# Optimization experiments

Measured on AMD Instinct MI355X. Metric: run time of the kernel, lower is better.

## Reference

```python
import jax, jax.numpy as jnp
import numpy as np

# model dims (see init_kwargs)
HID = 2048
H = 16
Q_LORA = 768
KV_LORA = 512
QK_NOPE = 128
QK_ROPE = 64
QK_HEAD = QK_NOPE + QK_ROPE  # 192
V_DIM = 128
HI = 8        # indexer heads
DI = 128      # indexer head dim
TOPK = 512    # index_topk
EPS = 1e-5
B, S = 1, 2048


def rms_norm(x, w):
    return x * jax.lax.rsqrt(jnp.mean(x * x, -1, keepdims=True) + EPS) * w


def layer_norm(x, w, b):
    m = jnp.mean(x, -1, keepdims=True)
    v = jnp.mean((x - m) ** 2, -1, keepdims=True)
    return (x - m) * jax.lax.rsqrt(v + EPS) * w + b


def rotate_half(x):
    x1, x2 = jnp.split(x, 2, axis=-1)
    return jnp.concatenate([-x2, x1], axis=-1)


def rope_bshd(x, cos, sin):
    # x: [B,S,H,D], cos/sin: [B,S,D] -> broadcast over heads (unsqueeze_dim=2)
    return x * cos[:, :, None, :] + rotate_half(x) * sin[:, :, None, :]


def setup_inputs() -> dict:
    key = jax.random.key(0)
    ks = jax.random.split(key, 16)
    std = 0.02
    hidden_states = jax.random.normal(ks[0], (B, S, HID), jnp.float32)
    # real RoPE tables, theta=10000, head_dim=QK_ROPE
    inv_freq = 1.0 / (10000.0 ** (np.arange(0, QK_ROPE, 2, dtype=np.float32) / QK_ROPE))
    freqs = np.arange(S, dtype=np.float32)[:, None] * inv_freq[None, :]  # [S, ROPE/2]
    emb = np.concatenate([freqs, freqs], axis=-1)
    cos = jnp.asarray(np.cos(emb))[None]  # [1,S,ROPE]
    sin = jnp.asarray(np.sin(emb))[None]
    w = lambda k, shp: jax.random.normal(k, shp, jnp.float32) * std
    return {
        'hidden_states': hidden_states, 'cos': cos, 'sin': sin,
        'wq_a': w(ks[1], (Q_LORA, HID)),
        'q_a_norm_w': jnp.ones((Q_LORA,), jnp.float32),
        'wq_b': w(ks[2], (H * QK_HEAD, Q_LORA)),
        'wkv_a': w(ks[3], (KV_LORA + QK_ROPE, HID)),
        'kv_a_norm_w': jnp.ones((KV_LORA,), jnp.float32),
        'wkv_b': w(ks[4], (H * (QK_NOPE + V_DIM), KV_LORA)),
        'wo': w(ks[5], (HID, H * V_DIM)),
        'idx_wq_b': w(ks[6], (HI * DI, Q_LORA)),
        'idx_wk': w(ks[7], (DI, HID)),
        'idx_k_norm_w': jnp.ones((DI,), jnp.float32),
        'idx_k_norm_b': jnp.zeros((DI,), jnp.float32),
        'idx_weights_w': w(ks[8], (HI, HID)),
    }


def reference(hidden_states, cos, sin, wq_a, q_a_norm_w, wq_b, wkv_a, kv_a_norm_w,
              wkv_b, wo, idx_wq_b, idx_wk, idx_k_norm_w, idx_k_norm_b, idx_weights_w):
    b, s, _ = hidden_states.shape
    # ---- MLA projections ----
    q_lora = rms_norm(hidden_states @ wq_a.T, q_a_norm_w)              # [B,S,Q_LORA]
    q = (q_lora @ wq_b.T).reshape(b, s, H, QK_HEAD)
    q_nope, q_rope = jnp.split(q, [QK_NOPE], axis=-1)
    q_rope = rope_bshd(q_rope, cos, sin)

    kv = hidden_states @ wkv_a.T                                        # [B,S,KV_LORA+ROPE]
    kv_lat, k_rope = jnp.split(kv, [KV_LORA], axis=-1)
    k_rope = k_rope * cos + rotate_half(k_rope) * sin                   # shared MQA rope key [B,S,ROPE]
    kv_lat = rms_norm(kv_lat, kv_a_norm_w)
    kvb = (kv_lat @ wkv_b.T).reshape(b, s, H, QK_NOPE + V_DIM)
    k_nope, value = jnp.split(kvb, [QK_NOPE], axis=-1)

    queries = jnp.concatenate([q_nope, q_rope], axis=-1)                # [B,S,H,QK_HEAD]
    keys = jnp.concatenate(
        [k_nope, jnp.broadcast_to(k_rope[:, :, None, :], (b, s, H, QK_ROPE))], axis=-1)

    # ---- lightning indexer (DSA): per-query top-k KV selection ----
    iq = (q_lora @ idx_wq_b.T).reshape(b, s, HI, DI)
    iq_rot, iq_pass = jnp.split(iq, [QK_ROPE], axis=-1)
    iq = jnp.concatenate([rope_bshd(iq_rot, cos, sin), iq_pass], axis=-1)
    ik = layer_norm(hidden_states @ idx_wk.T, idx_k_norm_w, idx_k_norm_b)  # [B,S,DI]
    ik_rot, ik_pass = jnp.split(ik, [QK_ROPE], axis=-1)
    ik = jnp.concatenate([ik_rot * cos + rotate_half(ik_rot) * sin, ik_pass], axis=-1)

    iscores = jnp.einsum('bqhd,bkd->bqhk', iq, ik) * (DI ** -0.5)       # [B,S,HI,S]
    iw = (hidden_states @ idx_weights_w.T) * (HI ** -0.5)               # [B,S,HI]
    iscore = jnp.einsum('bqh,bqhk->bqk', iw, iscores)                   # [B,S,S]

    causal = jnp.tril(jnp.ones((s, s), bool))
    iscore = jnp.where(causal[None], iscore, -1e9)
    _, topk_idx = jax.lax.top_k(iscore, TOPK)                           # [B,S,TOPK]
    allow = jnp.zeros((b, s, s), bool).at[
        jnp.arange(b)[:, None, None], jnp.arange(s)[None, :, None], topk_idx].set(True)
    allow = allow & causal[None]                                        # topk AND causal

    # ---- masked attention ----
    scale = QK_HEAD ** -0.5
    scores = jnp.einsum('bqhd,bkhd->bhqk', queries, keys) * scale       # [B,H,S,S]
    scores = jnp.where(allow[:, None], scores, -jnp.inf)
    probs = jax.nn.softmax(scores, axis=-1)
    out = jnp.einsum('bhqk,bkhd->bqhd', probs, value).reshape(b, s, H * V_DIM)
    return out @ wo.T
```

## Files before the change

kernel.cpp:

```cpp
#include <hip/hip_runtime.h>
#include <hip/hip_bf16.h>
#include <stdint.h>
#include <math.h>

#define S_LEN 2048
#define HIDDEN 2048
#define NHEAD 16
#define QLORA 768
#define KVLORA 512
#define QKNOPE 128
#define QKROPE 64
#define QKHEAD 192
#define VDIM 128
#define HIN 8
#define DIN 128
#define TOPKN 512
#define EPSF 1e-5f
#define DLAT 576
#define SCALE_ATT 0.07216878364870322f

typedef __bf16 bf16x8 __attribute__((ext_vector_type(8)));
typedef float  f32x4  __attribute__((ext_vector_type(4)));

static __device__ __forceinline__ float wave_reduce_sum(float v) {
    #pragma unroll
    for (int off = 32; off > 0; off >>= 1) v += __shfl_down(v, off);
    return v;
}

static __device__ __forceinline__ void splitw(__bf16* __restrict__ H,
                                              __bf16* __restrict__ L,
                                              size_t idx, float v) {
    __bf16 h = (__bf16)v;
    H[idx] = h;
    L[idx] = (__bf16)(v - (float)h);
}

static __device__ __forceinline__ void gll16(const __bf16* g, __bf16* lds_base) {
    __builtin_amdgcn_global_load_lds(
        (const __attribute__((address_space(1))) uint32_t*)g,
        (__attribute__((address_space(3))) uint32_t*)lds_base, 16, 0, 0);
}

#define PREP_BLOCKS 17280
__global__ __launch_bounds__(256) void prep_all(
        const float* __restrict__ hid,     __bf16* hidH,  __bf16* hidL,
        const float* __restrict__ wq_a,    __bf16* wqaH,  __bf16* wqaL,
        const float* __restrict__ idx_wq_b,__bf16* iwqH,  __bf16* iwqL,
        const float* __restrict__ idx_wk,  __bf16* iwkH,  __bf16* iwkL,
        const float* __restrict__ wq_b,    __bf16* wq_b_bf,
        const float* __restrict__ wkv_a,   __bf16* wkv_a_bf,
        const float* __restrict__ wkv_b,   __bf16* wkv_b_bf,
        const float* __restrict__ wo,      __bf16* wo_bf,
        __bf16* wknt) {
    int b = blockIdx.x, tid = threadIdx.x;
    const float* src; __bf16 *dH = nullptr, *dL = nullptr, *dC = nullptr;
    int base;
    if (b < 4096)        { src = hid;      dH = hidH; dL = hidL; base = b; }
    else if (b < 5632)   { src = wq_a;     dH = wqaH; dL = wqaL; base = b - 4096; }
    else if (b < 6400)   { src = idx_wq_b; dH = iwqH; dL = iwqL; base = b - 5632; }
    else if (b < 6656)   { src = idx_wk;   dH = iwkH; dL = iwkL; base = b - 6400; }
    else if (b < 8960)   { src = wq_b;     dC = wq_b_bf;  base = b - 6656; }
    else if (b < 10112)  { src = wkv_a;    dC = wkv_a_bf; base = b - 8960; }
    else if (b < 12160)  { src = wkv_b;    dC = wkv_b_bf; base = b - 10112; }
    else if (b < 16256)  { src = wo;       dC = wo_bf;    base = b - 12160; }
    else {
        int e = ((b - 16256) * 256 + tid) * 4;
        int c = e & 511, d = (e >> 9) & 127, h = e >> 16;
        f32x4 v = *(const f32x4*)(wkv_b + ((size_t)(h * 256 + d)) * 512 + c);
        #pragma unroll
        for (int j = 0; j < 4; ++j)
            wknt[(size_t)h * 65536 + (c + j) * 128 + d] = (__bf16)v[j];
        return;
    }
    int i = (base * 256 + tid) * 4;
    f32x4 v = *(const f32x4*)(src + i);
    if (dC) {
        #pragma unroll
        for (int j = 0; j < 4; ++j) dC[i + j] = (__bf16)v[j];
    } else {
        #pragma unroll
        for (int j = 0; j < 4; ++j) splitw(dH, dL, i + j, v[j]);
    }
}

#define GBM 128
#define GBN 64
#define GBK 32
template <typename OutT>
static __device__ __forceinline__ void gemm_s_core(
        const __bf16* __restrict__ A, const __bf16* __restrict__ B,
        OutT* __restrict__ C, int K, int lda, int ldb, int ldc,
        int bx, int by) {
    __shared__ __bf16 sAs[GBM * GBK];
    __shared__ __bf16 sBs[GBN * GBK];
    int tid = threadIdx.x;
    int lane = tid & 63, wid = tid >> 6;
    int quad = lane >> 4, l16 = lane & 15;
    int wm = wid >> 1, wn = wid & 1;
    int row0 = by * GBM, col0 = bx * GBN;
    int lr = lane >> 2, lk = (lane & 3) * 8;

    f32x4 acc[4][2] = {};

    for (int k0 = 0; k0 < K; k0 += GBK) {
        #pragma unroll
        for (int c = 0; c < 2; ++c) {
            int rb = (wid * 2 + c) * 16;
            gll16(A + (size_t)(row0 + rb + lr) * lda + k0 + lk, sAs + rb * GBK);
        }
        gll16(B + (size_t)(col0 + wid * 16 + lr) * ldb + k0 + lk, sBs + wid * 16 * GBK);
        __syncthreads();
        bf16x8 af[4], bfr[2];
        #pragma unroll
        for (int mi = 0; mi < 4; ++mi)
            af[mi] = *(const bf16x8*)&sAs[(wm * 64 + mi * 16 + l16) * GBK + quad * 8];
        #pragma unroll
        for (int ni = 0; ni < 2; ++ni)
            bfr[ni] = *(const bf16x8*)&sBs[(wn * 32 + ni * 16 + l16) * GBK + quad * 8];
        #pragma unroll
        for (int mi = 0; mi < 4; ++mi)
            #pragma unroll
            for (int ni = 0; ni < 2; ++ni)
                acc[mi][ni] = __builtin_amdgcn_mfma_f32_16x16x32_bf16(
                    af[mi], bfr[ni], acc[mi][ni], 0, 0, 0);
        __syncthreads();
    }
    #pragma unroll
    for (int mi = 0; mi < 4; ++mi)
        #pragma unroll
        for (int ni = 0; ni < 2; ++ni)
            #pragma unroll
            for (int r = 0; r < 4; ++r) {
                int row = row0 + wm * 64 + mi * 16 + quad * 4 + r;
                int col = col0 + wn * 32 + ni * 16 + l16;
                C[(size_t)row * ldc + col] = (OutT)acc[mi][ni][r];
            }
}

template <typename OutT>
__global__ __launch_bounds__(256) void gemm_s(const __bf16* __restrict__ A,
                                              const __bf16* __restrict__ B,
                                              OutT* __restrict__ C,
                                              int K, int lda, int ldb, int ldc,
                                              long sA, long sB, long sC) {
    gemm_s_core<OutT>(A + (size_t)blockIdx.z * sA, B + (size_t)blockIdx.z * sB,
                      C + (size_t)blockIdx.z * sC, K, lda, ldb, ldc,
                      blockIdx.x, blockIdx.y);
}

template <bool CAUSAL>
static __device__ __forceinline__ void gemm3_core(
        const __bf16* __restrict__ Ah, const __bf16* __restrict__ Al,
        const __bf16* __restrict__ Bh, const __bf16* __restrict__ Bl,
        float* __restrict__ C, int K, int lda, int ldb, int ldc,
        int row_base, int bx, int by) {
    int row0 = by * GBM + row_base, col0 = bx * GBN;
    if (CAUSAL && col0 > row0 + GBM - 1) return;
    __shared__ __bf16 sAh[GBM * GBK], sAl[GBM * GBK];
    __shared__ __bf16 sBh[GBN * GBK], sBl[GBN * GBK];
    int tid = threadIdx.x;
    int lane = tid & 63, wid = tid >> 6;
    int quad = lane >> 4, l16 = lane & 15;
    int wm = wid >> 1, wn = wid & 1;
    int lr = lane >> 2, lk = (lane & 3) * 8;

    f32x4 acc[4][2] = {};

    for (int k0 = 0; k0 < K; k0 += GBK) {
        #pragma unroll
        for (int c = 0; c < 2; ++c) {
            int rb = (wid * 2 + c) * 16;
            size_t go = (size_t)(row0 + rb + lr) * lda + k0 + lk;
            gll16(Ah + go, sAh + rb * GBK);
            gll16(Al + go, sAl + rb * GBK);
        }
        {
            size_t go = (size_t)(col0 + wid * 16 + lr) * ldb + k0 + lk;
            gll16(Bh + go, sBh + wid * 16 * GBK);
            gll16(Bl + go, sBl + wid * 16 * GBK);
        }
        __syncthreads();
        bf16x8 afh[4], afl[4], bfh[2], bfl[2];
        #pragma unroll
        for (int mi = 0; mi < 4; ++mi) {
            int o = (wm * 64 + mi * 16 + l16) * GBK + quad * 8;
            afh[mi] = *(const bf16x8*)&sAh[o];
            afl[mi] = *(const bf16x8*)&sAl[o];
        }
        #pragma unroll
        for (int ni = 0; ni < 2; ++ni) {
            int o = (wn * 32 + ni * 16 + l16) * GBK + quad * 8;
            bfh[ni] = *(const bf16x8*)&sBh[o];
            bfl[ni] = *(const bf16x8*)&sBl[o];
        }
        #pragma unroll
        for (int mi = 0; mi < 4; ++mi)
            #pragma unroll
            for (int ni = 0; ni < 2; ++ni) {
                acc[mi][ni] = __builtin_amdgcn_mfma_f32_16x16x32_bf16(
                    afl[mi], bfh[ni], acc[mi][ni], 0, 0, 0);
                acc[mi][ni] = __builtin_amdgcn_mfma_f32_16x16x32_bf16(
                    afh[mi], bfl[ni], acc[mi][ni], 0, 0, 0);
                acc[mi][ni] = __builtin_amdgcn_mfma_f32_16x16x32_bf16(
                    afh[mi], bfh[ni], acc[mi][ni], 0, 0, 0);
            }
        __syncthreads();
    }
    #pragma unroll
    for (int mi = 0; mi < 4; ++mi)
        #pragma unroll
        for (int ni = 0; ni < 2; ++ni)
            #pragma unroll
            for (int r = 0; r < 4; ++r) {
                int row = row0 + wm * 64 + mi * 16 + quad * 4 + r;
                int col = col0 + wn * 32 + ni * 16 + l16;
                C[(size_t)row * ldc + col] = acc[mi][ni][r];
            }
}

__global__ __launch_bounds__(256) void gemm3_ks(const __bf16* __restrict__ Ah,
                                                const __bf16* __restrict__ Al,
                                                const __bf16* __restrict__ Bh,
                                                const __bf16* __restrict__ Bl,
                                                float* __restrict__ Cpart,
                                                int Ksub, int lda, int ldb, int ldc,
                                                long sC) {
    int bz = blockIdx.z, koff = bz * Ksub;
    gemm3_core<false>(Ah + koff, Al + koff, Bh + koff, Bl + koff,
                      Cpart + (size_t)bz * sC, Ksub, lda, ldb, ldc, 0,
                      blockIdx.x, blockIdx.y);
}

__global__ __launch_bounds__(256) void fused_mid(
        const __bf16* __restrict__ qlH, const __bf16* __restrict__ qlL,
        const __bf16* __restrict__ wq_b_bf, __bf16* __restrict__ qbuf_bf,
        const __bf16* __restrict__ hidH, const __bf16* __restrict__ hidL,
        const __bf16* __restrict__ wkv_a_bf, float* __restrict__ kv,
        const __bf16* __restrict__ iwqH, const __bf16* __restrict__ iwqL,
        float* __restrict__ iqraw,
        const __bf16* __restrict__ iwkH, const __bf16* __restrict__ iwkL,
        float* __restrict__ ikraw) {
    int b = blockIdx.x;
    if (b < 768) {
        gemm_s_core<__bf16>(qlH, wq_b_bf, qbuf_bf, QLORA, QLORA, QLORA,
                            NHEAD * QKHEAD, b % 48, b / 48);
    } else if (b < 912) {
        int r = b - 768;
        gemm_s_core<float>(hidH, wkv_a_bf, kv, HIDDEN, HIDDEN, HIDDEN, DLAT,
                           r % 9, r / 9);
    } else if (b < 1168) {
        int r = b - 912;
        gemm3_core<false>(qlH, qlL, iwqH, iwqL, iqraw, QLORA, QLORA, QLORA,
                          HIN * DIN, 0, r & 15, r >> 4);
    } else {
        int r = b - 1168;
        gemm3_core<false>(hidH, hidL, iwkH, iwkL, ikraw, HIDDEN, HIDDEN, HIDDEN,
                          DIN, 0, r & 1, r >> 1);
    }
}

__global__ __launch_bounds__(256) void fused2(
        const __bf16* __restrict__ qbuf_bf, const __bf16* __restrict__ wknt,
        __bf16* __restrict__ qeff,
        const __bf16* __restrict__ cqH, const __bf16* __restrict__ cqL,
        const __bf16* __restrict__ ikH, const __bf16* __restrict__ ikL,
        float* __restrict__ iscore) {
    int b = blockIdx.x;
    if (b < 2048) {
        int bx = b & 7, by = (b >> 3) & 15, bz = b >> 7;
        gemm_s_core<__bf16>(qbuf_bf + bz * QKHEAD, wknt + (size_t)bz * 512 * 128,
                            qeff + bz * DLAT, 128, NHEAD * QKHEAD, 128,
                            NHEAD * DLAT, bx, by);
    } else {
        int r = b - 2048;
        gemm3_core<true>(cqH, cqL, ikH, ikL, iscore, DIN, DIN, DIN, S_LEN,
                         TOPKN, r & 31, r >> 5);
    }
}

__global__ __launch_bounds__(256) void rmsnorm_split4(const float* __restrict__ p,
                                                      long ps,
                                                      const float* __restrict__ w,
                                                      __bf16* __restrict__ yH,
                                                      __bf16* __restrict__ yL, int ncols) {
    int row = blockIdx.x, tid = threadIdx.x;
    const float* p0 = p + (size_t)row * ncols;
    float ss = 0.f;
    for (int c = tid; c < ncols; c += 256) {
        float v = p0[c] + p0[ps + c] + p0[2 * ps + c] + p0[3 * ps + c];
        ss += v * v;
    }
    __shared__ float red[4];
    ss = wave_reduce_sum(ss);
    if ((tid & 63) == 0) red[tid >> 6] = ss;
    __syncthreads();
    float tot = red[0] + red[1] + red[2] + red[3];
    float inv = rsqrtf(tot / (float)ncols + EPSF);
    for (int c = tid; c < ncols; c += 256) {
        float v = p0[c] + p0[ps + c] + p0[2 * ps + c] + p0[3 * ps + c];
        splitw(yH, yL, (size_t)row * ncols + c, v * inv * w[c]);
    }
}

__global__ __launch_bounds__(256) void fused_post(
        const __bf16* __restrict__ qbuf, __bf16* __restrict__ qeff,
        const float* __restrict__ kv, const float* __restrict__ kvw,
        __bf16* __restrict__ klat,
        const float* __restrict__ ikraw, const float* __restrict__ lnw,
        const float* __restrict__ lnb, __bf16* __restrict__ ikH, __bf16* __restrict__ ikL,
        const float* __restrict__ iqraw, const float* __restrict__ hid,
        const float* __restrict__ iww, __bf16* __restrict__ cqH, __bf16* __restrict__ cqL,
        const float* __restrict__ cosT, const float* __restrict__ sinT) {
    int s = blockIdx.x, tid = threadIdx.x;
    int lane = tid & 63, wid = tid >> 6;

    for (int i = tid; i < NHEAD * 32; i += 256) {
        int h = i >> 5, d = i & 31;
        const __bf16* base = qbuf + (size_t)s * (NHEAD * QKHEAD) + h * QKHEAD + QKNOPE;
        float x1 = (float)base[d], x2 = (float)base[d + 32];
        float c1 = cosT[s * 64 + d],      s1 = sinT[s * 64 + d];
        float c2 = cosT[s * 64 + d + 32], s2 = sinT[s * 64 + d + 32];
        __bf16* o = qeff + (size_t)s * (NHEAD * DLAT) + h * DLAT + 512;
        o[d]      = (__bf16)(x1 * c1 - x2 * s1);
        o[d + 32] = (__bf16)(x2 * c2 + x1 * s2);
    }

    {
        const float* row = kv + (size_t)s * DLAT;
        float ss = 0.f;
        for (int c = tid; c < KVLORA; c += 256) { float v = row[c]; ss += v * v; }
        __shared__ float redB[4];
        ss = wave_reduce_sum(ss);
        if (lane == 0) redB[wid] = ss;
        __syncthreads();
        float tot = redB[0] + redB[1] + redB[2] + redB[3];
        float inv = rsqrtf(tot / (float)KVLORA + EPSF);
        __bf16* orow = klat + (size_t)s * DLAT;
        for (int c = tid; c < KVLORA; c += 256)
            orow[c] = (__bf16)(row[c] * inv * kvw[c]);
        if (tid < 32) {
            int d = tid;
            float x1 = row[KVLORA + d], x2 = row[KVLORA + d + 32];
            float c1 = cosT[s * 64 + d],      s1 = sinT[s * 64 + d];
            float c2 = cosT[s * 64 + d + 32], s2 = sinT[s * 64 + d + 32];
            orow[512 + d]      = (__bf16)(x1 * c1 - x2 * s1);
            orow[512 + d + 32] = (__bf16)(x2 * c2 + x1 * s2);
        }
    }

    {
        float x = (tid < DIN) ? ikraw[(size_t)s * DIN + tid] : 0.f;
        __shared__ float redC1[4], redC2[4], sy[DIN];
        float sm = wave_reduce_sum(x);
        if (lane == 0) redC1[wid] = sm;
        __syncthreads();
        float mean = (redC1[0] + redC1[1] + redC1[2] + redC1[3]) / (float)DIN;
        float dx = (tid < DIN) ? (x - mean) : 0.f;
        float vs = wave_reduce_sum(dx * dx);
        if (lane == 0) redC2[wid] = vs;
        __syncthreads();
        float var = (redC2[0] + redC2[1] + redC2[2] + redC2[3]) / (float)DIN;
        if (tid < DIN) sy[tid] = dx * rsqrtf(var + EPSF) * lnw[tid] + lnb[tid];
        __syncthreads();
        size_t ro = (size_t)s * DIN;
        if (tid < 32) {
            int d = tid;
            float c1 = cosT[s * 64 + d],      s1 = sinT[s * 64 + d];
            float c2 = cosT[s * 64 + d + 32], s2 = sinT[s * 64 + d + 32];
            splitw(ikH, ikL, ro + d,      sy[d] * c1 - sy[d + 32] * s1);
            splitw(ikH, ikL, ro + d + 32, sy[d + 32] * c2 + sy[d] * s2);
        } else if (tid >= 64 && tid < DIN) {
            splitw(ikH, ikL, ro + tid, sy[tid]);
        }
        __syncthreads();
    }

    {
        __shared__ float redD[4][HIN], siw[HIN];
        float a8[HIN] = {};
        const float* xr = hid + (size_t)s * HIDDEN;
        for (int c = tid; c < HIDDEN; c += 256) {
            float x = xr[c];
            #pragma unroll
            for (int h = 0; h < HIN; ++h) a8[h] += x * iww[h * HIDDEN + c];
        }
        #pragma unroll
        for (int h = 0; h < HIN; ++h) a8[h] = wave_reduce_sum(a8[h]);
        if (lane == 0)
            #pragma unroll
            for (int h = 0; h < HIN; ++h) redD[wid][h] = a8[h];
        __syncthreads();
        if (tid < HIN)
            siw[tid] = redD[0][tid] + redD[1][tid] + redD[2][tid] + redD[3][tid];
        __syncthreads();
        if (tid < DIN) {
            int d = tid;
            float acc = 0.f;
            float c1 = 0.f, s1 = 0.f;
            if (d < 64) { c1 = cosT[s * 64 + d]; s1 = sinT[s * 64 + d]; }
            #pragma unroll
            for (int h = 0; h < HIN; ++h) {
                const float* base = iqraw + ((size_t)s * HIN + h) * DIN;
                float v;
                if (d < 32)       v = base[d] * c1 - base[d + 32] * s1;
                else if (d < 64)  v = base[d] * c1 + base[d - 32] * s1;
                else              v = base[d];
                acc += siw[h] * v;
            }
            splitw(cqH, cqL, (size_t)s * DIN + d, acc * 0.03125f);
        }
    }
}

__global__ __launch_bounds__(256) void topk_rows(const float* __restrict__ iscore,
                                                 int* __restrict__ topk) {
    int q = TOPKN + blockIdx.x;
    int n = q + 1;
    __shared__ uint32_t skey[S_LEN];
    __shared__ int hist[256];
    __shared__ int scan[256];
    __shared__ uint32_t sp;
    __shared__ int sr, pos;
    int tid = threadIdx.x;
    const float* row = iscore + (size_t)q * S_LEN;
    for (int i = tid; i < n; i += 256) {
        uint32_t u = __float_as_uint(row[i]);
        skey[i] = (u & 0x80000000u) ? ~u : (u | 0x80000000u);
    }
    __syncthreads();
    uint32_t prefix = 0;
    int remk = TOPKN;
    for (int pass = 0; pass < 4; ++pass) {
        int shift = 24 - 8 * pass;
        uint32_t pmask = pass ? (0xFFFFFFFFu << (shift + 8)) : 0u;
        hist[tid] = 0;
        __syncthreads();
        for (int i = tid; i < n; i += 256) {
            uint32_t u = skey[i];
            if ((u & pmask) == prefix) atomicAdd(&hist[(u >> shift) & 255], 1);
        }
        __syncthreads();
        scan[tid] = hist[tid];
        __syncthreads();
        for (int step = 1; step < 256; step <<= 1) {
            int v = (tid + step < 256) ? scan[tid + step] : 0;
            __syncthreads();
            scan[tid] += v;
            __syncthreads();
        }
        int Sb = scan[tid];
        int Snext = (tid < 255) ? scan[tid + 1] : 0;
        if (Sb >= remk && Snext < remk) {
            sp = prefix | ((uint32_t)tid << shift);
            sr = remk - Snext;
        }
        __syncthreads();
        prefix = sp; remk = sr;
        __syncthreads();
    }
    if (tid == 0) pos = 0;
    __syncthreads();
    int* orow = topk + (size_t)q * TOPKN;
    for (int i = tid; i < n; i += 256) {
        if (skey[i] > prefix) { int p = atomicAdd(&pos, 1); orow[p] = i; }
    }
    __syncthreads();
    int base = pos;
    int chunk = (n + 255) >> 8;
    int lo = tid * chunk, hiEnd = lo + chunk;
    if (hiEnd > n) hiEnd = n;
    int cnt = 0;
    for (int i = lo; i < hiEnd; ++i) cnt += (skey[i] == prefix);
    scan[tid] = cnt;
    __syncthreads();
    for (int step = 1; step < 256; step <<= 1) {
        int v = (tid >= step) ? scan[tid - step] : 0;
        __syncthreads();
        scan[tid] += v;
        __syncthreads();
    }
    int r = scan[tid] - cnt;
    for (int i = lo; i < hiEnd && r < remk; ++i) {
        if (skey[i] == prefix) { orow[base + r] = i; ++r; }
    }
}

__global__ __launch_bounds__(256) void attn2(const __bf16* __restrict__ qeff,
                                             const __bf16* __restrict__ klat,
                                             const int* __restrict__ topk,
                                             __bf16* __restrict__ o_lat) {
    int q = (blockIdx.x * 997) & (S_LEN - 1);
    int tid = threadIdx.x;
    int lane = tid & 63, wid = tid >> 6;
    int l16 = lane & 15, quad = lane >> 4;
    int wn = wid & 1, wk = wid >> 1;

    __shared__ int   s_gk[2][32];
    __shared__ float s_part[2][16][37];
    __shared__ float s_S[16][40];
    __shared__ float s_m[16], s_l[16], s_alpha[16], s_inv[16];

    int L = (q < TOPKN) ? (q + 1) : TOPKN;
    int nt = (L + 31) >> 5;
    const int* idxr = topk + (size_t)q * TOPKN;

    bf16x8 qf[9];
    const __bf16* qrow = qeff + (size_t)q * (NHEAD * DLAT) + l16 * DLAT + wk * 288 + quad * 8;
    #pragma unroll
    for (int s = 0; s < 9; ++s) qf[s] = *(const bf16x8*)(qrow + s * 32);

    if (tid < 16) { s_m[tid] = -1e30f; s_l[tid] = 0.f; }

    f32x4 oacc[8];
    #pragma unroll
    for (int i = 0; i < 8; ++i) oacc[i] = (f32x4){0.f, 0.f, 0.f, 0.f};

    for (int t = 0; t < nt; ++t) {
        if (tid < 32) {
            int ki = t * 32 + tid;
            int gk = 0;
            if (ki < L) gk = (q < TOPKN) ? ki : idxr[ki];
            s_gk[t & 1][tid] = gk;
        }
        __syncthreads();

        int myk = s_gk[t & 1][wn * 16 + l16];
        const __bf16* krow = klat + (size_t)myk * DLAT + wk * 288 + quad * 8;
        f32x4 sacc = {0.f, 0.f, 0.f, 0.f};
        #pragma unroll
        for (int s = 0; s < 9; ++s) {
            bf16x8 kf = *(const bf16x8*)(krow + s * 32);
            sacc = __builtin_amdgcn_mfma_f32_16x16x32_bf16(qf[s], kf, sacc, 0, 0, 0);
        }
        #pragma unroll
        for (int r = 0; r < 4; ++r)
            s_part[wk][quad * 4 + r][wn * 16 + l16] = sacc[r];
        __syncthreads();

        {
            int h = tid >> 4, k0 = (tid & 15) * 2;
            float v0 = -1e30f, v1 = -1e30f;
            if (t * 32 + k0 < L)
                v0 = (s_part[0][h][k0] + s_part[1][h][k0]) * SCALE_ATT;
            if (t * 32 + k0 + 1 < L)
                v1 = (s_part[0][h][k0 + 1] + s_part[1][h][k0 + 1]) * SCALE_ATT;
            float mt = fmaxf(v0, v1);
            #pragma unroll
            for (int o = 1; o < 16; o <<= 1) mt = fmaxf(mt, __shfl_xor(mt, o));
            float mold = s_m[h];
            float mnew = fmaxf(mold, mt);
            float p0 = __expf(v0 - mnew), p1 = __expf(v1 - mnew);
            float ls = p0 + p1;
            #pragma unroll
            for (int o = 1; o < 16; o <<= 1) ls += __shfl_xor(ls, o);
            *(float2*)&s_S[h][k0] = make_float2(p0, p1);
            if ((tid & 15) == 0) {
                float alpha = __expf(mold - mnew);
                s_alpha[h] = alpha;
                s_m[h] = mnew;
                s_l[h] = s_l[h] * alpha + ls;
            }
        }
        __syncthreads();

        f32x4 al4 = *(const f32x4*)&s_alpha[quad * 4];
        f32x4 p0v = *(const f32x4*)&s_S[l16][quad * 8];
        f32x4 p1v = *(const f32x4*)&s_S[l16][quad * 8 + 4];
        bf16x8 pf;
        #pragma unroll
        for (int i = 0; i < 4; ++i) {
            pf[i]     = (__bf16)p0v[i];
            pf[4 + i] = (__bf16)p1v[i];
        }
        const __bf16* vb[8];
        #pragma unroll
        for (int j = 0; j < 8; ++j)
            vb[j] = klat + (size_t)s_gk[t & 1][quad * 8 + j] * DLAT;
        #pragma unroll
        for (int n = 0; n < 8; ++n) {
            int dim = wid * 128 + n * 16 + l16;
            bf16x8 vf;
            #pragma unroll
            for (int j = 0; j < 8; ++j) vf[j] = vb[j][dim];
            #pragma unroll
            for (int r = 0; r < 4; ++r) oacc[n][r] *= al4[r];
            oacc[n] = __builtin_amdgcn_mfma_f32_16x16x32_bf16(pf, vf, oacc[n], 0, 0, 0);
        }
    }

    if (tid < 16) s_inv[tid] = 1.f / s_l[tid];
    __syncthreads();
    f32x4 inv4 = *(const f32x4*)&s_inv[quad * 4];
    #pragma unroll
    for (int n = 0; n < 8; ++n) {
        int dim = wid * 128 + n * 16 + l16;
        #pragma unroll
        for (int r = 0; r < 4; ++r) {
            int h = quad * 4 + r;
            o_lat[(size_t)q * 8192 + h * 512 + dim] = (__bf16)(oacc[n][r] * inv4[r]);
        }
    }
}

extern "C" void kernel_launch(void* const* d_in, const int* in_sizes, int n_in,
                              void* d_out, int out_size, void* d_ws, size_t ws_size,
                              hipStream_t stream) {
    const float* hid          = (const float*)d_in[0];
    const float* cosT         = (const float*)d_in[1];
    const float* sinT         = (const float*)d_in[2];
    const float* wq_a         = (const float*)d_in[3];
    const float* q_a_norm_w   = (const float*)d_in[4];
    const float* wq_b         = (const float*)d_in[5];
    const float* wkv_a        = (const float*)d_in[6];
    const float* kv_a_norm_w  = (const float*)d_in[7];
    const float* wkv_b        = (const float*)d_in[8];
    const float* wo           = (const float*)d_in[9];
    const float* idx_wq_b     = (const float*)d_in[10];
    const float* idx_wk       = (const float*)d_in[11];
    const float* idx_k_norm_w = (const float*)d_in[12];
    const float* idx_k_norm_b = (const float*)d_in[13];
    const float* idx_weights_w= (const float*)d_in[14];
    float* out = (float*)d_out;

    char* ws = (char*)d_ws;
    size_t off = 0;
    auto alloc = [&](size_t nbytes) {
        void* p = (void*)(ws + off);
        off += (nbytes + 255) & ~(size_t)255;
        return p;
    };
    __bf16* qbuf_bf  = (__bf16*)alloc((size_t)S_LEN * NHEAD * QKHEAD * 2);
    float*  kv       = (float*) alloc((size_t)S_LEN * DLAT * 4);
    __bf16* klat_bf  = (__bf16*)alloc((size_t)S_LEN * DLAT * 2);
    __bf16* qeff_bf  = (__bf16*)alloc((size_t)S_LEN * NHEAD * DLAT * 2);
    int*    topk     = (int*)   alloc((size_t)S_LEN * TOPKN * 4);
    char* uB = (char*)alloc((size_t)S_LEN * HIDDEN * 2 + (size_t)DLAT * HIDDEN * 2);
    __bf16* hidH      = (__bf16*)uB;
    __bf16* wkv_a_bf  = (__bf16*)(uB + (size_t)S_LEN * HIDDEN * 2);
    __bf16* attn_o_bf = (__bf16*)uB;
    __bf16* hidL      = (__bf16*)alloc((size_t)S_LEN * HIDDEN * 2);
    char* uC = (char*)alloc((size_t)S_LEN * NHEAD * 512 * 2);
    float*  qpart    = (float*)uC;
    __bf16* o_lat_bf = (__bf16*)uC;
    float* iqraw  = (float*)uC;
    float* ikraw  = (float*)(uC + 8388608);
    float* iscore = (float*)(uC + 11599872);
    __bf16* wq_b_bf  = (__bf16*)alloc((size_t)(NHEAD * QKHEAD) * QLORA * 2);
    __bf16* wkv_b_bf = (__bf16*)alloc((size_t)(NHEAD * 256) * KVLORA * 2);
    __bf16* wknt_bf  = (__bf16*)alloc((size_t)NHEAD * 512 * 128 * 2);
    __bf16* wo_bf    = (__bf16*)alloc((size_t)HIDDEN * (NHEAD * VDIM) * 2);
    __bf16* wqaH = (__bf16*)alloc((size_t)QLORA * HIDDEN * 2);
    __bf16* wqaL = (__bf16*)alloc((size_t)QLORA * HIDDEN * 2);
    __bf16* qlH  = (__bf16*)alloc((size_t)S_LEN * QLORA * 2);
    __bf16* qlL  = (__bf16*)alloc((size_t)S_LEN * QLORA * 2);
    __bf16* iwqH = (__bf16*)alloc((size_t)(HIN * DIN) * QLORA * 2);
    __bf16* iwqL = (__bf16*)alloc((size_t)(HIN * DIN) * QLORA * 2);
    __bf16* iwkH = (__bf16*)alloc((size_t)DIN * HIDDEN * 2);
    __bf16* iwkL = (__bf16*)alloc((size_t)DIN * HIDDEN * 2);
    __bf16* ikH  = (__bf16*)alloc((size_t)S_LEN * DIN * 2);
    __bf16* ikL  = (__bf16*)alloc((size_t)S_LEN * DIN * 2);
    __bf16* cqH  = (__bf16*)alloc((size_t)S_LEN * DIN * 2);
    __bf16* cqL  = (__bf16*)alloc((size_t)S_LEN * DIN * 2);
    (void)ws_size; (void)in_sizes; (void)n_in; (void)out_size;

    dim3 blk(256);

    prep_all<<<PREP_BLOCKS, blk, 0, stream>>>(
        hid, hidH, hidL, wq_a, wqaH, wqaL, idx_wq_b, iwqH, iwqL,
        idx_wk, iwkH, iwkL, wq_b, wq_b_bf, wkv_a, wkv_a_bf,
        wkv_b, wkv_b_bf, wo, wo_bf, wknt_bf);

    gemm3_ks<<<dim3(QLORA / GBN, S_LEN / GBM, 4), blk, 0, stream>>>(
        hidH, hidL, wqaH, wqaL, qpart, HIDDEN / 4, HIDDEN, HIDDEN, QLORA,
        (long)S_LEN * QLORA);
    rmsnorm_split4<<<S_LEN, 256, 0, stream>>>(qpart, (long)S_LEN * QLORA,
                                              q_a_norm_w, qlH, qlL, QLORA);

    fused_mid<<<1200, blk, 0, stream>>>(qlH, qlL, wq_b_bf, qbuf_bf,
                                        hidH, hidL, wkv_a_bf, kv,
                                        iwqH, iwqL, iqraw, iwkH, iwkL, ikraw);

    fused_post<<<S_LEN, 256, 0, stream>>>(qbuf_bf, qeff_bf, kv, kv_a_norm_w, klat_bf,
                                          ikraw, idx_k_norm_w, idx_k_norm_b, ikH, ikL,
                                          iqraw, hid, idx_weights_w, cqH, cqL,
                                          cosT, sinT);

    fused2<<<2048 + 384, blk, 0, stream>>>(qbuf_bf, wknt_bf, qeff_bf,
                                           cqH, cqL, ikH, ikL, iscore);

    topk_rows<<<S_LEN - TOPKN, 256, 0, stream>>>(iscore, topk);

    attn2<<<S_LEN, 256, 0, stream>>>(qeff_bf, klat_bf, topk, o_lat_bf);

    gemm_s<__bf16><<<dim3(VDIM / GBN, S_LEN / GBM, NHEAD), blk, 0, stream>>>(
        o_lat_bf, wkv_b_bf + 128 * 512, attn_o_bf, 512,
        NHEAD * 512, 512, NHEAD * VDIM, 512, 256 * 512, VDIM);
    gemm_s<float><<<dim3(HIDDEN / GBN, S_LEN / GBM, 1), blk, 0, stream>>>(
        attn_o_bf, wo_bf, out, NHEAD * VDIM,
        NHEAD * VDIM, NHEAD * VDIM, HIDDEN, 0, 0, 0);
}
```

Measured before the change: 620.7 us.

## Stage gathered latent V rows in LDS and vectorize PV operand loads

```diff
diff --git a/kernel.cpp b/kernel.cpp
--- a/kernel.cpp
+++ b/kernel.cpp
@@ -20,6 +20,7 @@
 #define SCALE_ATT 0.07216878364870322f
 
 typedef __bf16 bf16x8 __attribute__((ext_vector_type(8)));
+typedef __bf16 bf16x4 __attribute__((ext_vector_type(4)));
 typedef float  f32x4  __attribute__((ext_vector_type(4)));
 
 static __device__ __forceinline__ float wave_reduce_sum(float v) {
@@ -486,6 +487,7 @@
     }
 }
 
+#define SVP 520
 __global__ __launch_bounds__(256) void attn2(const __bf16* __restrict__ qeff,
                                              const __bf16* __restrict__ klat,
                                              const int* __restrict__ topk,
@@ -496,8 +498,9 @@
     int l16 = lane & 15, quad = lane >> 4;
     int wn = wid & 1, wk = wid >> 1;
 
+    __shared__ short sV[32 * SVP];
     __shared__ int   s_gk[2][32];
-    __shared__ float s_part[2][16][37];
+    __shared__ float s_part[2][16][33];
     __shared__ float s_S[16][40];
     __shared__ float s_m[16], s_l[16], s_alpha[16], s_inv[16];
 
@@ -515,6 +518,8 @@
     f32x4 oacc[8];
     #pragma unroll
     for (int i = 0; i < 8; ++i) oacc[i] = (f32x4){0.f, 0.f, 0.f, 0.f};
+
+    int srow = tid >> 3, schk = tid & 7;
 
     for (int t = 0; t < nt; ++t) {
         if (tid < 32) {
@@ -524,6 +529,14 @@
             s_gk[t & 1][tid] = gk;
         }
         __syncthreads();
+
+        {
+            int gk = s_gk[t & 1][srow];
+            const uint4* src = (const uint4*)(klat + (size_t)gk * DLAT) + schk * 8;
+            uint4* dst = (uint4*)((char*)sV + srow * (SVP * 2) + schk * 128);
+            #pragma unroll
+            for (int c = 0; c < 8; ++c) dst[c] = src[c];
+        }
 
         int myk = s_gk[t & 1][wn * 16 + l16];
         const __bf16* krow = klat + (size_t)myk * DLAT + wk * 288 + quad * 8;
@@ -565,27 +578,36 @@
         __syncthreads();
 
         f32x4 al4 = *(const f32x4*)&s_alpha[quad * 4];
-        f32x4 p0v = *(const f32x4*)&s_S[l16][quad * 8];
-        f32x4 p1v = *(const f32x4*)&s_S[l16][quad * 8 + 4];
         bf16x8 pf;
-        #pragma unroll
-        for (int i = 0; i < 4; ++i) {
-            pf[i]     = (__bf16)p0v[i];
-            pf[4 + i] = (__bf16)p1v[i];
-        }
-        const __bf16* vb[8];
-        #pragma unroll
-        for (int j = 0; j < 8; ++j)
-            vb[j] = klat + (size_t)s_gk[t & 1][quad * 8 + j] * DLAT;
-        #pragma unroll
-        for (int n = 0; n < 8; ++n) {
-            int dim = wid * 128 + n * 16 + l16;
-            bf16x8 vf;
-            #pragma unroll
-            for (int j = 0; j < 8; ++j) vf[j] = vb[j][dim];
-            #pragma unroll
-            for (int r = 0; r < 4; ++r) oacc[n][r] *= al4[r];
-            oacc[n] = __builtin_amdgcn_mfma_f32_16x16x32_bf16(pf, vf, oacc[n], 0, 0, 0);
+        int qhi = quad & 2, qlo = quad & 1;
+        #pragma unroll
+        for (int p = 0; p < 4; ++p) {
+            float2 v = *(const float2*)&s_S[l16][quad * 8 + ((2 * p) ^ qhi)];
+            float e0 = qlo ? v.y : v.x, e1 = qlo ? v.x : v.y;
+            pf[2 * p]     = (__bf16)e0;
+            pf[2 * p + 1] = (__bf16)e1;
+        }
+        const __bf16* sVb = (const __bf16*)sV;
+        #pragma unroll
+        for (int g = 0; g < 2; ++g) {
+            int dbase = wid * 128 + g * 64;
+            bf16x8 vf[4];
+            #pragma unroll
+            for (int j = 0; j < 8; ++j) {
+                int j2 = j ^ quad;
+                bf16x4 v4 = *(const bf16x4*)&sVb[(quad * 8 + j2) * SVP + dbase + 4 * l16];
+                vf[0][j] = v4[0];
+                vf[1][j] = v4[1];
+                vf[2][j] = v4[2];
+                vf[3][j] = v4[3];
+            }
+            #pragma unroll
+            for (int m = 0; m < 4; ++m) {
+                int i = g * 4 + m;
+                #pragma unroll
+                for (int r = 0; r < 4; ++r) oacc[i][r] *= al4[r];
+                oacc[i] = __builtin_amdgcn_mfma_f32_16x16x32_bf16(pf, vf[m], oacc[i], 0, 0, 0);
+            }
         }
     }
 
@@ -593,14 +615,17 @@
     __syncthreads();
     f32x4 inv4 = *(const f32x4*)&s_inv[quad * 4];
     #pragma unroll
-    for (int n = 0; n < 8; ++n) {
-        int dim = wid * 128 + n * 16 + l16;
+    for (int g = 0; g < 2; ++g)
         #pragma unroll
         for (int r = 0; r < 4; ++r) {
             int h = quad * 4 + r;
-            o_lat[(size_t)q * 8192 + h * 512 + dim] = (__bf16)(oacc[n][r] * inv4[r]);
-        }
-    }
+            bf16x4 w;
+            #pragma unroll
+            for (int m = 0; m < 4; ++m)
+                w[m] = (__bf16)(oacc[g * 4 + m][r] * inv4[r]);
+            *(bf16x4*)(o_lat + (size_t)q * 8192 + h * 512 +
+                       wid * 128 + g * 64 + 4 * l16) = w;
+        }
 }
 
 extern "C" void kernel_launch(void* const* d_in, const int* in_sizes, int n_in,
```

After: 740.5 us. 1.19x slower.

## Stage gathered latent K rows in shared memory for QK and PV

Applied to the files above, without the earlier changes.

```diff
diff --git a/kernel.cpp b/kernel.cpp
--- a/kernel.cpp
+++ b/kernel.cpp
@@ -486,6 +486,7 @@
     }
 }
 
+#define SKS 584
 __global__ __launch_bounds__(256) void attn2(const __bf16* __restrict__ qeff,
                                              const __bf16* __restrict__ klat,
                                              const int* __restrict__ topk,
@@ -496,9 +497,9 @@
     int l16 = lane & 15, quad = lane >> 4;
     int wn = wid & 1, wk = wid >> 1;
 
-    __shared__ int   s_gk[2][32];
+    __shared__ short sK[32 * SKS];
     __shared__ float s_part[2][16][37];
-    __shared__ float s_S[16][40];
+    __shared__ float s_S[16][38];
     __shared__ float s_m[16], s_l[16], s_alpha[16], s_inv[16];
 
     int L = (q < TOPKN) ? (q + 1) : TOPKN;
@@ -516,21 +517,23 @@
     #pragma unroll
     for (int i = 0; i < 8; ++i) oacc[i] = (f32x4){0.f, 0.f, 0.f, 0.f};
 
+    int srow = tid >> 3, schk = tid & 7;
+
     for (int t = 0; t < nt; ++t) {
-        if (tid < 32) {
-            int ki = t * 32 + tid;
-            int gk = 0;
-            if (ki < L) gk = (q < TOPKN) ? ki : idxr[ki];
-            s_gk[t & 1][tid] = gk;
-        }
-        __syncthreads();
-
-        int myk = s_gk[t & 1][wn * 16 + l16];
-        const __bf16* krow = klat + (size_t)myk * DLAT + wk * 288 + quad * 8;
+        int ki = t * 32 + srow;
+        int gk = 0;
+        if (ki < L) gk = (q < TOPKN) ? ki : idxr[ki];
+        const uint4* src = (const uint4*)(klat + (size_t)gk * DLAT) + schk * 9;
+        uint4* dst = (uint4*)((char*)sK + srow * (SKS * 2) + schk * 144);
+        #pragma unroll
+        for (int c = 0; c < 9; ++c) dst[c] = src[c];
+        __syncthreads();
+
         f32x4 sacc = {0.f, 0.f, 0.f, 0.f};
+        const short* kbase = sK + (wn * 16 + l16) * SKS + wk * 288 + quad * 8;
         #pragma unroll
         for (int s = 0; s < 9; ++s) {
-            bf16x8 kf = *(const bf16x8*)(krow + s * 32);
+            bf16x8 kf = *(const bf16x8*)(kbase + s * 32);
             sacc = __builtin_amdgcn_mfma_f32_16x16x32_bf16(qf[s], kf, sacc, 0, 0, 0);
         }
         #pragma unroll
@@ -565,28 +568,28 @@
         __syncthreads();
 
         f32x4 al4 = *(const f32x4*)&s_alpha[quad * 4];
-        f32x4 p0v = *(const f32x4*)&s_S[l16][quad * 8];
-        f32x4 p1v = *(const f32x4*)&s_S[l16][quad * 8 + 4];
         bf16x8 pf;
-        #pragma unroll
-        for (int i = 0; i < 4; ++i) {
-            pf[i]     = (__bf16)p0v[i];
-            pf[4 + i] = (__bf16)p1v[i];
-        }
-        const __bf16* vb[8];
-        #pragma unroll
-        for (int j = 0; j < 8; ++j)
-            vb[j] = klat + (size_t)s_gk[t & 1][quad * 8 + j] * DLAT;
+        int qhi = quad & 2, qlo = quad & 1;
+        #pragma unroll
+        for (int p = 0; p < 4; ++p) {
+            float2 v = *(const float2*)&s_S[l16][quad * 8 + ((2 * p) ^ qhi)];
+            float e0 = qlo ? v.y : v.x, e1 = qlo ? v.x : v.y;
+            pf[2 * p]     = (__bf16)e0;
+            pf[2 * p + 1] = (__bf16)e1;
+        }
+        const __bf16* sKb = (const __bf16*)sK;
         #pragma unroll
         for (int n = 0; n < 8; ++n) {
             int dim = wid * 128 + n * 16 + l16;
             bf16x8 vf;
             #pragma unroll
-            for (int j = 0; j < 8; ++j) vf[j] = vb[j][dim];
+            for (int j = 0; j < 8; ++j)
+                vf[j] = sKb[(quad * 8 + (j ^ quad)) * SKS + dim];
             #pragma unroll
             for (int r = 0; r < 4; ++r) oacc[n][r] *= al4[r];
             oacc[n] = __builtin_amdgcn_mfma_f32_16x16x32_bf16(pf, vf, oacc[n], 0, 0, 0);
         }
+        __syncthreads();
     }
 
     if (tid < 16) s_inv[tid] = 1.f / s_l[tid];
```

Result: faster. 559.0 us (-9.9%).
